# Kernel tuning notes

Measured on AMD Instinct MI355X. Metric: run time of the kernel, lower is better.

## Reference

```python
import jax, jax.numpy as jnp
import numpy as np

D_MODEL = 1024
NUM_HEADS = 16
D_K = D_MODEL // NUM_HEADS


def setup_inputs() -> dict:
    key = jax.random.key(0)
    ks = jax.random.split(key, 11)
    B, S = 4, 2048
    s = 1.0 / np.sqrt(D_MODEL)
    return {
        "query": jax.random.normal(ks[0], (B, S, D_MODEL), jnp.float32),
        "key_in": jax.random.normal(ks[1], (B, S, D_MODEL), jnp.float32),
        "value": jax.random.normal(ks[2], (B, S, D_MODEL), jnp.float32),
        "Wq": jax.random.normal(ks[3], (D_MODEL, D_MODEL), jnp.float32) * s,
        "bq": jnp.zeros((D_MODEL,), jnp.float32),
        "Wk": jax.random.normal(ks[4], (D_MODEL, D_MODEL), jnp.float32) * s,
        "bk": jnp.zeros((D_MODEL,), jnp.float32),
        "Wv": jax.random.normal(ks[5], (D_MODEL, D_MODEL), jnp.float32) * s,
        "bv": jnp.zeros((D_MODEL,), jnp.float32),
        "Wo": jax.random.normal(ks[6], (D_MODEL, D_MODEL), jnp.float32) * s,
        "bo": jnp.zeros((D_MODEL,), jnp.float32),
    }


def _split_heads(x):
    # (B, S, d_model) -> (B, H, S, d_k)
    B, S, _ = x.shape
    return x.reshape(B, S, NUM_HEADS, D_K).transpose(0, 2, 1, 3)


def reference(query, key_in, value, Wq, bq, Wk, bk, Wv, bv, Wo, bo):
    # Linear projections (torch nn.Linear: x @ W.T + b)
    Q = _split_heads(query @ Wq.T + bq)   # (B, H, Sq, d_k)
    K = _split_heads(key_in @ Wk.T + bk)  # (B, H, Sk, d_k)
    V = _split_heads(value @ Wv.T + bv)   # (B, H, Sk, d_k)
    # Scaled dot-product attention (mask=None path)
    scores = jnp.einsum('bhqd,bhkd->bhqk', Q, K) / jnp.sqrt(jnp.float32(D_K))
    attn = jax.nn.softmax(scores, axis=-1)
    out = jnp.einsum('bhqk,bhkd->bhqd', attn, V)  # (B, H, Sq, d_k)
    B, H, Sq, _ = out.shape
    out = out.transpose(0, 2, 1, 3).reshape(B, Sq, D_MODEL)
    return out @ Wo.T + bo
```

## Files before the change

kernel.cpp:

```cpp
#include <hip/hip_runtime.h>


#define DMODEL 1024
#define DK     64
#define NH     16
#define BSZ    4
#define SEQ    2048
#define MTOT   (BSZ * SEQ)

typedef __attribute__((ext_vector_type(8))) __bf16 bf16x8;
typedef __attribute__((ext_vector_type(4))) float  f32x4;

__device__ inline unsigned short f2bf(float x) {
    union { float f; unsigned u; } v; v.f = x;
    unsigned r = v.u + 0x7FFF + ((v.u >> 16) & 1u);
    return (unsigned short)(r >> 16);
}

__device__ inline bf16x8 ld_frag(const unsigned short* p) {
    return __builtin_bit_cast(bf16x8, *(const int4*)p);
}

union V8 { int4 v; unsigned short s[8]; };

__device__ inline void gload16(const unsigned short* g, unsigned short* l) {
    __builtin_amdgcn_global_load_lds(
        (const __attribute__((address_space(1))) void*)g,
        (__attribute__((address_space(3))) void*)l, 16, 0, 0);
}

__device__ inline unsigned pack_bf(float lo, float hi) {
    unsigned b0 = __builtin_bit_cast(unsigned, lo) + 0x8000u;
    unsigned b1 = __builtin_bit_cast(unsigned, hi) + 0x8000u;
    return __builtin_amdgcn_perm(b1, b0, 0x07060302u);
}

__global__ __launch_bounds__(256)
void conv_bf16(const float* __restrict__ src, unsigned short* __restrict__ dst)
{
    int i = blockIdx.x * 256 + threadIdx.x;
    const float4* s = (const float4*)src + (size_t)i * 2;
    float4 a = s[0], b = s[1];
    V8 u;
    u.s[0] = f2bf(a.x); u.s[1] = f2bf(a.y); u.s[2] = f2bf(a.z); u.s[3] = f2bf(a.w);
    u.s[4] = f2bf(b.x); u.s[5] = f2bf(b.y); u.s[6] = f2bf(b.z); u.s[7] = f2bf(b.w);
    ((int4*)dst)[i] = u.v;
}

template<int OUT_F32, int BIAS_ROW>
__global__ __launch_bounds__(256)
void gemm_bt16(const unsigned short* __restrict__ A, const unsigned short* __restrict__ Bt,
               const float* __restrict__ bias, void* __restrict__ Cout,
               int Mdim, int Ndim, int Kdim, float scale)
{
    __shared__ unsigned short As[128 * 64];
    __shared__ unsigned short Bs[128 * 64];

    const int tid  = threadIdx.x;
    const int wave = tid >> 6, lane = tid & 63, quad = lane >> 4, l16 = lane & 15;
    const int wm = wave >> 1, wn = wave & 1;
    const int m0 = blockIdx.x * 128, n0 = blockIdx.y * 128;

    const int srow = lane >> 3;
    const int pch  = lane & 7;

    f32x4 acc[4][4];
#pragma unroll
    for (int i = 0; i < 4; ++i)
#pragma unroll
        for (int j = 0; j < 4; ++j)
#pragma unroll
            for (int r = 0; r < 4; ++r) acc[i][j][r] = 0.f;

    for (int k0 = 0; k0 < Kdim; k0 += 64) {
#pragma unroll
        for (int rr = 0; rr < 4; ++rr) {
            int row = rr * 32 + wave * 8 + srow;
            int c   = pch ^ (row & 7);
            gload16(A + (size_t)(m0 + row) * Kdim + k0 + c * 8,
                    &As[(size_t)(rr * 32 + wave * 8) * 64]);
        }
#pragma unroll
        for (int rr = 0; rr < 4; ++rr) {
            int row = rr * 32 + wave * 8 + srow;
            int c   = pch ^ (row & 7);
            gload16(Bt + (size_t)(n0 + row) * Kdim + k0 + c * 8,
                    &Bs[(size_t)(rr * 32 + wave * 8) * 64]);
        }
        __syncthreads();

#pragma unroll
        for (int hh = 0; hh < 2; ++hh) {
            bf16x8 af[4], bfr[4];
#pragma unroll
            for (int t = 0; t < 4; ++t) {
                int ra = wm * 64 + t * 16 + l16;
                int pa = (hh * 4 + quad) ^ (l16 & 7);
                af[t] = ld_frag(&As[(size_t)ra * 64 + pa * 8]);
                int rb = wn * 64 + t * 16 + l16;
                bfr[t] = ld_frag(&Bs[(size_t)rb * 64 + pa * 8]);
            }
#pragma unroll
            for (int i = 0; i < 4; ++i)
#pragma unroll
                for (int j = 0; j < 4; ++j)
                    acc[i][j] = __builtin_amdgcn_mfma_f32_16x16x32_bf16(af[i], bfr[j], acc[i][j], 0, 0, 0);
        }
        __syncthreads();
    }

#pragma unroll
    for (int j = 0; j < 4; ++j) {
        int n = n0 + wn * 64 + j * 16 + l16;
        float bcol = BIAS_ROW ? 0.f : bias[n];
#pragma unroll
        for (int i = 0; i < 4; ++i) {
#pragma unroll
            for (int r = 0; r < 4; ++r) {
                int m = m0 + wm * 64 + i * 16 + quad * 4 + r;
                float bv = BIAS_ROW ? bias[m] : bcol;
                float val = (acc[i][j][r] + bv) * scale;
                if (OUT_F32) ((float*)Cout)[(size_t)m * Ndim + n] = val;
                else ((unsigned short*)Cout)[(size_t)m * Ndim + n] = f2bf(val);
            }
        }
    }
}

__global__ __launch_bounds__(256)
void attn_kernel(const unsigned short* __restrict__ Qb, const unsigned short* __restrict__ Kb,
                 const unsigned short* __restrict__ VbT, unsigned short* __restrict__ Ob)
{
    __shared__ unsigned short Ks[64 * 64];
    __shared__ unsigned short Vt[64 * 64];
    __shared__ unsigned short Ps[4][32][72];

    const int tid  = threadIdx.x;
    const int wave = tid >> 6, lane = tid & 63, quad = lane >> 4, l16 = lane & 15;
    const int q0 = blockIdx.x * 128, h = blockIdx.y, b = blockIdx.z;
    const int sw = l16 & 7;

    bf16x8 qf[2][2];
    const unsigned short* qbase = Qb + (size_t)(b * SEQ + q0 + wave * 32) * DMODEL + h * DK;
#pragma unroll
    for (int qs = 0; qs < 2; ++qs)
#pragma unroll
        for (int hh = 0; hh < 2; ++hh)
            qf[qs][hh] = ld_frag(qbase + (size_t)(qs * 16 + l16) * DMODEL + hh * 32 + quad * 8);

    f32x4 zero4;
#pragma unroll
    for (int r = 0; r < 4; ++r) zero4[r] = 0.f;

    f32x4 o[2][4], lacc[2];
#pragma unroll
    for (int qs = 0; qs < 2; ++qs) {
        lacc[qs] = zero4;
#pragma unroll
        for (int t = 0; t < 4; ++t) o[qs][t] = zero4;
    }

    bf16x8 onesf;
    {
        V8 u;
#pragma unroll
        for (int j = 0; j < 8; ++j) u.s[j] = 0x3F80;
        onesf = __builtin_bit_cast(bf16x8, u.v);
    }

    const int sr  = lane >> 3;
    const int pch = lane & 7;

    for (int kt = 0; kt < SEQ; kt += 64) {
        __syncthreads();
#pragma unroll
        for (int i = 0; i < 2; ++i) {
            int blk = wave * 2 + i;
            int row = blk * 8 + sr;
            int c   = pch ^ (row & 7);
            int key = 4 * (row & 15) + (row >> 4);
            gload16(Kb + (size_t)(b * SEQ + kt + key) * DMODEL + h * DK + c * 8,
                    &Ks[(size_t)blk * 512]);
            gload16(VbT + (size_t)(h * DK + row) * MTOT + b * SEQ + kt + c * 8,
                    &Vt[(size_t)blk * 512]);
        }
        __syncthreads();

        f32x4 s[2][4];
#pragma unroll
        for (int c = 0; c < 4; ++c) {
            bf16x8 kb0 = ld_frag(&Ks[(size_t)(c * 16 + l16) * 64 + ((quad ^ sw) * 8)]);
            bf16x8 kb1 = ld_frag(&Ks[(size_t)(c * 16 + l16) * 64 + (((4 + quad) ^ sw) * 8)]);
            s[0][c] = __builtin_amdgcn_mfma_f32_16x16x32_bf16(qf[0][1], kb1,
                      __builtin_amdgcn_mfma_f32_16x16x32_bf16(qf[0][0], kb0, zero4, 0, 0, 0), 0, 0, 0);
            s[1][c] = __builtin_amdgcn_mfma_f32_16x16x32_bf16(qf[1][1], kb1,
                      __builtin_amdgcn_mfma_f32_16x16x32_bf16(qf[1][0], kb0, zero4, 0, 0, 0), 0, 0, 0);
        }

#pragma unroll
        for (int qs = 0; qs < 2; ++qs)
#pragma unroll
            for (int r = 0; r < 4; ++r) {
                float p0 = __builtin_amdgcn_exp2f(s[qs][0][r]);
                float p1 = __builtin_amdgcn_exp2f(s[qs][1][r]);
                float p2 = __builtin_amdgcn_exp2f(s[qs][2][r]);
                float p3 = __builtin_amdgcn_exp2f(s[qs][3][r]);
                uint2 pk;
                pk.x = pack_bf(p0, p1);
                pk.y = pack_bf(p2, p3);
                *(uint2*)&Ps[wave][qs * 16 + quad * 4 + r][4 * l16] = pk;
            }

        bf16x8 pf[2][2];
#pragma unroll
        for (int qs = 0; qs < 2; ++qs)
#pragma unroll
            for (int hh = 0; hh < 2; ++hh)
                pf[qs][hh] = ld_frag(&Ps[wave][qs * 16 + l16][hh * 32 + quad * 8]);

#pragma unroll
        for (int qs = 0; qs < 2; ++qs) {
            lacc[qs] = __builtin_amdgcn_mfma_f32_16x16x32_bf16(pf[qs][0], onesf, lacc[qs], 0, 0, 0);
            lacc[qs] = __builtin_amdgcn_mfma_f32_16x16x32_bf16(pf[qs][1], onesf, lacc[qs], 0, 0, 0);
        }

#pragma unroll
        for (int t = 0; t < 4; ++t)
#pragma unroll
            for (int hh = 0; hh < 2; ++hh) {
                bf16x8 vb = ld_frag(&Vt[(size_t)(t * 16 + l16) * 64 + (((hh * 4 + quad) ^ sw) * 8)]);
                o[0][t] = __builtin_amdgcn_mfma_f32_16x16x32_bf16(pf[0][hh], vb, o[0][t], 0, 0, 0);
                o[1][t] = __builtin_amdgcn_mfma_f32_16x16x32_bf16(pf[1][hh], vb, o[1][t], 0, 0, 0);
            }
    }

#pragma unroll
    for (int qs = 0; qs < 2; ++qs) {
        float inv[4];
#pragma unroll
        for (int r = 0; r < 4; ++r) inv[r] = 1.f / lacc[qs][r];
#pragma unroll
        for (int t = 0; t < 4; ++t) {
            int d = h * DK + t * 16 + l16;
#pragma unroll
            for (int r = 0; r < 4; ++r) {
                int q = q0 + wave * 32 + qs * 16 + quad * 4 + r;
                Ob[(size_t)(b * SEQ + q) * DMODEL + d] = f2bf(o[qs][t][r] * inv[r]);
            }
        }
    }
}

extern "C" void kernel_launch(void* const* d_in, const int* in_sizes, int n_in,
                              void* d_out, int out_size, void* d_ws, size_t ws_size,
                              hipStream_t stream)
{
    const float* query  = (const float*)d_in[0];
    const float* key_in = (const float*)d_in[1];
    const float* value  = (const float*)d_in[2];
    const float* Wq = (const float*)d_in[3];
    const float* bq = (const float*)d_in[4];
    const float* Wk = (const float*)d_in[5];
    const float* bk = (const float*)d_in[6];
    const float* Wv = (const float*)d_in[7];
    const float* bv = (const float*)d_in[8];
    const float* Wo = (const float*)d_in[9];
    const float* bo = (const float*)d_in[10];

    const size_t NM = (size_t)MTOT * DMODEL;
    const size_t NW = (size_t)DMODEL * DMODEL;
    unsigned short* tmpA = (unsigned short*)d_ws;
    unsigned short* tmpW = tmpA + NM;
    unsigned short* Qb   = tmpW + NW;
    unsigned short* Kb   = Qb + NM;
    unsigned short* VbT  = Kb + NM;
    unsigned short* Ob   = tmpA;

    dim3 bb(256);
    const int gcA = (int)(NM / 8 / 256);
    const int gcW = (int)(NW / 8 / 256);
    dim3 gg(MTOT / 128, DMODEL / 128);
    dim3 gv(DMODEL / 128, MTOT / 128);

    const float qscale = 0.18033688f;

    conv_bf16<<<gcA, bb, 0, stream>>>(query, tmpA);
    conv_bf16<<<gcW, bb, 0, stream>>>(Wq, tmpW);
    gemm_bt16<0, 0><<<gg, bb, 0, stream>>>(tmpA, tmpW, bq, Qb, MTOT, DMODEL, DMODEL, qscale);

    conv_bf16<<<gcA, bb, 0, stream>>>(key_in, tmpA);
    conv_bf16<<<gcW, bb, 0, stream>>>(Wk, tmpW);
    gemm_bt16<0, 0><<<gg, bb, 0, stream>>>(tmpA, tmpW, bk, Kb, MTOT, DMODEL, DMODEL, 1.0f);

    conv_bf16<<<gcA, bb, 0, stream>>>(value, tmpA);
    conv_bf16<<<gcW, bb, 0, stream>>>(Wv, tmpW);
    gemm_bt16<0, 1><<<gv, bb, 0, stream>>>(tmpW, tmpA, bv, VbT, DMODEL, MTOT, DMODEL, 1.0f);

    attn_kernel<<<dim3(SEQ / 128, NH, BSZ), bb, 0, stream>>>(Qb, Kb, VbT, Ob);

    conv_bf16<<<gcW, bb, 0, stream>>>(Wo, tmpW);
    gemm_bt16<1, 0><<<gg, bb, 0, stream>>>(Ob, tmpW, bo, d_out, MTOT, DMODEL, DMODEL, 1.0f);
}
```

Baseline: 368.3 us.

## Batch QKV projections and conversions into single launches, retile output GEMM

Converts all three activations and all four weights to bf16 in two batched launches, keeping separate workspace buffers for each. The three projection GEMMs then run as one launch with blockIdx.z choosing Q, K or V, so 1536 blocks are in flight instead of 512 per launch. The output projection uses a 64x128 tile, giving twice as many blocks for better CU fill. This needs more workspace, so a fallback path keeps the old sequential launches when the workspace is too small.

```diff
diff --git a/kernel.cpp b/kernel.cpp
--- a/kernel.cpp
+++ b/kernel.cpp
@@ -35,10 +35,9 @@
     return __builtin_amdgcn_perm(b1, b0, 0x07060302u);
 }
 
-__global__ __launch_bounds__(256)
-void conv_bf16(const float* __restrict__ src, unsigned short* __restrict__ dst)
-{
-    int i = blockIdx.x * 256 + threadIdx.x;
+__device__ inline void conv_body(const float* __restrict__ src,
+                                 unsigned short* __restrict__ dst, int i)
+{
     const float4* s = (const float4*)src + (size_t)i * 2;
     float4 a = s[0], b = s[1];
     V8 u;
@@ -47,6 +46,35 @@
     ((int4*)dst)[i] = u.v;
 }
 
+__global__ __launch_bounds__(256)
+void conv_bf16(const float* __restrict__ src, unsigned short* __restrict__ dst)
+{
+    conv_body(src, dst, blockIdx.x * 256 + threadIdx.x);
+}
+
+__global__ __launch_bounds__(256)
+void conv3(const float* __restrict__ s0, const float* __restrict__ s1,
+           const float* __restrict__ s2, unsigned short* __restrict__ d0,
+           unsigned short* __restrict__ d1, unsigned short* __restrict__ d2)
+{
+    int z = blockIdx.z;
+    const float* s = (z == 0) ? s0 : (z == 1) ? s1 : s2;
+    unsigned short* d = (z == 0) ? d0 : (z == 1) ? d1 : d2;
+    conv_body(s, d, blockIdx.x * 256 + threadIdx.x);
+}
+
+__global__ __launch_bounds__(256)
+void conv4(const float* __restrict__ s0, const float* __restrict__ s1,
+           const float* __restrict__ s2, const float* __restrict__ s3,
+           unsigned short* __restrict__ d0, unsigned short* __restrict__ d1,
+           unsigned short* __restrict__ d2, unsigned short* __restrict__ d3)
+{
+    int z = blockIdx.z;
+    const float* s = (z == 0) ? s0 : (z == 1) ? s1 : (z == 2) ? s2 : s3;
+    unsigned short* d = (z == 0) ? d0 : (z == 1) ? d1 : (z == 2) ? d2 : d3;
+    conv_body(s, d, blockIdx.x * 256 + threadIdx.x);
+}
+
 template<int OUT_F32, int BIAS_ROW>
 __global__ __launch_bounds__(256)
 void gemm_bt16(const unsigned short* __restrict__ A, const unsigned short* __restrict__ Bt,
@@ -60,9 +88,7 @@
     const int wave = tid >> 6, lane = tid & 63, quad = lane >> 4, l16 = lane & 15;
     const int wm = wave >> 1, wn = wave & 1;
     const int m0 = blockIdx.x * 128, n0 = blockIdx.y * 128;
-
-    const int srow = lane >> 3;
-    const int pch  = lane & 7;
+    const int srow = lane >> 3, pch = lane & 7;
 
     f32x4 acc[4][4];
 #pragma unroll
@@ -122,6 +148,172 @@
                 float val = (acc[i][j][r] + bv) * scale;
                 if (OUT_F32) ((float*)Cout)[(size_t)m * Ndim + n] = val;
                 else ((unsigned short*)Cout)[(size_t)m * Ndim + n] = f2bf(val);
+            }
+        }
+    }
+}
+
+__global__ __launch_bounds__(256)
+void qkv_gemm(const unsigned short* __restrict__ Qa, const unsigned short* __restrict__ Ka,
+              const unsigned short* __restrict__ Va,
+              const unsigned short* __restrict__ Wqb, const unsigned short* __restrict__ Wkb,
+              const unsigned short* __restrict__ Wvb,
+              const float* __restrict__ bq, const float* __restrict__ bk,
+              const float* __restrict__ bv,
+              unsigned short* __restrict__ Qb, unsigned short* __restrict__ Kb,
+              unsigned short* __restrict__ VbT, float qscale)
+{
+    __shared__ unsigned short As[128 * 64];
+    __shared__ unsigned short Bs[128 * 64];
+
+    const int z = blockIdx.z;
+    const unsigned short* A  = (z == 0) ? Qa  : (z == 1) ? Ka  : Wvb;
+    const unsigned short* Bt = (z == 0) ? Wqb : (z == 1) ? Wkb : Va;
+    const float* bias        = (z == 0) ? bq  : (z == 1) ? bk  : bv;
+    unsigned short* out      = (z == 0) ? Qb  : (z == 1) ? Kb  : VbT;
+    const float scale  = (z == 0) ? qscale : 1.0f;
+    const int brow     = (z == 2);
+    const int m0       = brow ? blockIdx.y * 128 : blockIdx.x * 128;
+    const int n0       = brow ? blockIdx.x * 128 : blockIdx.y * 128;
+    const int ostride  = brow ? MTOT : DMODEL;
+
+    const int tid  = threadIdx.x;
+    const int wave = tid >> 6, lane = tid & 63, quad = lane >> 4, l16 = lane & 15;
+    const int wm = wave >> 1, wn = wave & 1;
+    const int srow = lane >> 3, pch = lane & 7;
+
+    f32x4 acc[4][4];
+#pragma unroll
+    for (int i = 0; i < 4; ++i)
+#pragma unroll
+        for (int j = 0; j < 4; ++j)
+#pragma unroll
+            for (int r = 0; r < 4; ++r) acc[i][j][r] = 0.f;
+
+    for (int k0 = 0; k0 < DMODEL; k0 += 64) {
+#pragma unroll
+        for (int rr = 0; rr < 4; ++rr) {
+            int row = rr * 32 + wave * 8 + srow;
+            int c   = pch ^ (row & 7);
+            gload16(A + (size_t)(m0 + row) * DMODEL + k0 + c * 8,
+                    &As[(size_t)(rr * 32 + wave * 8) * 64]);
+        }
+#pragma unroll
+        for (int rr = 0; rr < 4; ++rr) {
+            int row = rr * 32 + wave * 8 + srow;
+            int c   = pch ^ (row & 7);
+            gload16(Bt + (size_t)(n0 + row) * DMODEL + k0 + c * 8,
+                    &Bs[(size_t)(rr * 32 + wave * 8) * 64]);
+        }
+        __syncthreads();
+
+#pragma unroll
+        for (int hh = 0; hh < 2; ++hh) {
+            bf16x8 af[4], bfr[4];
+#pragma unroll
+            for (int t = 0; t < 4; ++t) {
+                int ra = wm * 64 + t * 16 + l16;
+                int pa = (hh * 4 + quad) ^ (l16 & 7);
+                af[t] = ld_frag(&As[(size_t)ra * 64 + pa * 8]);
+                int rb = wn * 64 + t * 16 + l16;
+                bfr[t] = ld_frag(&Bs[(size_t)rb * 64 + pa * 8]);
+            }
+#pragma unroll
+            for (int i = 0; i < 4; ++i)
+#pragma unroll
+                for (int j = 0; j < 4; ++j)
+                    acc[i][j] = __builtin_amdgcn_mfma_f32_16x16x32_bf16(af[i], bfr[j], acc[i][j], 0, 0, 0);
+        }
+        __syncthreads();
+    }
+
+#pragma unroll
+    for (int j = 0; j < 4; ++j) {
+        int n = n0 + wn * 64 + j * 16 + l16;
+        float bcol = brow ? 0.f : bias[n];
+#pragma unroll
+        for (int i = 0; i < 4; ++i) {
+#pragma unroll
+            for (int r = 0; r < 4; ++r) {
+                int m = m0 + wm * 64 + i * 16 + quad * 4 + r;
+                float bvv = brow ? bias[m] : bcol;
+                out[(size_t)m * ostride + n] = f2bf((acc[i][j][r] + bvv) * scale);
+            }
+        }
+    }
+}
+
+__global__ __launch_bounds__(256)
+void out_gemm(const unsigned short* __restrict__ A, const unsigned short* __restrict__ Bt,
+              const float* __restrict__ bias, float* __restrict__ C)
+{
+    __shared__ unsigned short As[64 * 64];
+    __shared__ unsigned short Bs[128 * 64];
+
+    const int tid  = threadIdx.x;
+    const int wave = tid >> 6, lane = tid & 63, quad = lane >> 4, l16 = lane & 15;
+    const int wm = wave >> 1, wn = wave & 1;
+    const int m0 = blockIdx.x * 64, n0 = blockIdx.y * 128;
+    const int srow = lane >> 3, pch = lane & 7;
+
+    f32x4 acc[2][4];
+#pragma unroll
+    for (int i = 0; i < 2; ++i)
+#pragma unroll
+        for (int j = 0; j < 4; ++j)
+#pragma unroll
+            for (int r = 0; r < 4; ++r) acc[i][j][r] = 0.f;
+
+    for (int k0 = 0; k0 < DMODEL; k0 += 64) {
+#pragma unroll
+        for (int rr = 0; rr < 2; ++rr) {
+            int row = rr * 32 + wave * 8 + srow;
+            int c   = pch ^ (row & 7);
+            gload16(A + (size_t)(m0 + row) * DMODEL + k0 + c * 8,
+                    &As[(size_t)(rr * 32 + wave * 8) * 64]);
+        }
+#pragma unroll
+        for (int rr = 0; rr < 4; ++rr) {
+            int row = rr * 32 + wave * 8 + srow;
+            int c   = pch ^ (row & 7);
+            gload16(Bt + (size_t)(n0 + row) * DMODEL + k0 + c * 8,
+                    &Bs[(size_t)(rr * 32 + wave * 8) * 64]);
+        }
+        __syncthreads();
+
+#pragma unroll
+        for (int hh = 0; hh < 2; ++hh) {
+            bf16x8 af[2], bfr[4];
+            int pa_base = hh * 4 + quad;
+#pragma unroll
+            for (int t = 0; t < 2; ++t) {
+                int ra = wm * 32 + t * 16 + l16;
+                af[t] = ld_frag(&As[(size_t)ra * 64 + ((pa_base ^ (l16 & 7)) * 8)]);
+            }
+#pragma unroll
+            for (int t = 0; t < 4; ++t) {
+                int rb = wn * 64 + t * 16 + l16;
+                bfr[t] = ld_frag(&Bs[(size_t)rb * 64 + ((pa_base ^ (l16 & 7)) * 8)]);
+            }
+#pragma unroll
+            for (int i = 0; i < 2; ++i)
+#pragma unroll
+                for (int j = 0; j < 4; ++j)
+                    acc[i][j] = __builtin_amdgcn_mfma_f32_16x16x32_bf16(af[i], bfr[j], acc[i][j], 0, 0, 0);
+        }
+        __syncthreads();
+    }
+
+#pragma unroll
+    for (int j = 0; j < 4; ++j) {
+        int n = n0 + wn * 64 + j * 16 + l16;
+        float bcol = bias[n];
+#pragma unroll
+        for (int i = 0; i < 2; ++i) {
+#pragma unroll
+            for (int r = 0; r < 4; ++r) {
+                int m = m0 + wm * 32 + i * 16 + quad * 4 + r;
+                C[(size_t)m * DMODEL + n] = acc[i][j][r] + bcol;
             }
         }
     }
@@ -269,35 +461,61 @@
 
     const size_t NM = (size_t)MTOT * DMODEL;
     const size_t NW = (size_t)DMODEL * DMODEL;
-    unsigned short* tmpA = (unsigned short*)d_ws;
-    unsigned short* tmpW = tmpA + NM;
-    unsigned short* Qb   = tmpW + NW;
-    unsigned short* Kb   = Qb + NM;
-    unsigned short* VbT  = Kb + NM;
-    unsigned short* Ob   = tmpA;
-
+    const float qscale = 0.18033688f;
     dim3 bb(256);
-    const int gcA = (int)(NM / 8 / 256);
-    const int gcW = (int)(NW / 8 / 256);
-    dim3 gg(MTOT / 128, DMODEL / 128);
-    dim3 gv(DMODEL / 128, MTOT / 128);
-
-    const float qscale = 0.18033688f;
-
-    conv_bf16<<<gcA, bb, 0, stream>>>(query, tmpA);
-    conv_bf16<<<gcW, bb, 0, stream>>>(Wq, tmpW);
-    gemm_bt16<0, 0><<<gg, bb, 0, stream>>>(tmpA, tmpW, bq, Qb, MTOT, DMODEL, DMODEL, qscale);
-
-    conv_bf16<<<gcA, bb, 0, stream>>>(key_in, tmpA);
-    conv_bf16<<<gcW, bb, 0, stream>>>(Wk, tmpW);
-    gemm_bt16<0, 0><<<gg, bb, 0, stream>>>(tmpA, tmpW, bk, Kb, MTOT, DMODEL, DMODEL, 1.0f);
-
-    conv_bf16<<<gcA, bb, 0, stream>>>(value, tmpA);
-    conv_bf16<<<gcW, bb, 0, stream>>>(Wv, tmpW);
-    gemm_bt16<0, 1><<<gv, bb, 0, stream>>>(tmpW, tmpA, bv, VbT, DMODEL, MTOT, DMODEL, 1.0f);
-
-    attn_kernel<<<dim3(SEQ / 128, NH, BSZ), bb, 0, stream>>>(Qb, Kb, VbT, Ob);
-
-    conv_bf16<<<gcW, bb, 0, stream>>>(Wo, tmpW);
-    gemm_bt16<1, 0><<<gg, bb, 0, stream>>>(Ob, tmpW, bo, d_out, MTOT, DMODEL, DMODEL, 1.0f);
-}
+
+    const size_t need_primary = (6 * NM + 4 * NW) * 2;
+
+    if (ws_size >= need_primary) {
+        unsigned short* Qa  = (unsigned short*)d_ws;
+        unsigned short* Ka  = Qa + NM;
+        unsigned short* Va  = Ka + NM;
+        unsigned short* Qb  = Va + NM;
+        unsigned short* Kb  = Qb + NM;
+        unsigned short* VbT = Kb + NM;
+        unsigned short* Wqb = VbT + NM;
+        unsigned short* Wkb = Wqb + NW;
+        unsigned short* Wvb = Wkb + NW;
+        unsigned short* Wob = Wvb + NW;
+        unsigned short* Ob  = Qa;
+
+        conv3<<<dim3(4096, 1, 3), bb, 0, stream>>>(query, key_in, value, Qa, Ka, Va);
+        conv4<<<dim3(512, 1, 4), bb, 0, stream>>>(Wq, Wk, Wv, Wo, Wqb, Wkb, Wvb, Wob);
+
+        qkv_gemm<<<dim3(MTOT / 128, DMODEL / 128, 3), bb, 0, stream>>>(
+            Qa, Ka, Va, Wqb, Wkb, Wvb, bq, bk, bv, Qb, Kb, VbT, qscale);
+
+        attn_kernel<<<dim3(SEQ / 128, NH, BSZ), bb, 0, stream>>>(Qb, Kb, VbT, Ob);
+
+        out_gemm<<<dim3(MTOT / 64, DMODEL / 128), bb, 0, stream>>>(Ob, Wob, bo, (float*)d_out);
+    } else {
+        unsigned short* tmpA = (unsigned short*)d_ws;
+        unsigned short* tmpW = tmpA + NM;
+        unsigned short* Qb   = tmpW + NW;
+        unsigned short* Kb   = Qb + NM;
+        unsigned short* VbT  = Kb + NM;
+        unsigned short* Ob   = tmpA;
+
+        const int gcA = (int)(NM / 8 / 256);
+        const int gcW = (int)(NW / 8 / 256);
+        dim3 gg(MTOT / 128, DMODEL / 128);
+        dim3 gv(DMODEL / 128, MTOT / 128);
+
+        conv_bf16<<<gcA, bb, 0, stream>>>(query, tmpA);
+        conv_bf16<<<gcW, bb, 0, stream>>>(Wq, tmpW);
+        gemm_bt16<0, 0><<<gg, bb, 0, stream>>>(tmpA, tmpW, bq, Qb, MTOT, DMODEL, DMODEL, qscale);
+
+        conv_bf16<<<gcA, bb, 0, stream>>>(key_in, tmpA);
+        conv_bf16<<<gcW, bb, 0, stream>>>(Wk, tmpW);
+        gemm_bt16<0, 0><<<gg, bb, 0, stream>>>(tmpA, tmpW, bk, Kb, MTOT, DMODEL, DMODEL, 1.0f);
+
+        conv_bf16<<<gcA, bb, 0, stream>>>(value, tmpA);
+        conv_bf16<<<gcW, bb, 0, stream>>>(Wv, tmpW);
+        gemm_bt16<0, 1><<<gv, bb, 0, stream>>>(tmpW, tmpA, bv, VbT, DMODEL, MTOT, DMODEL, 1.0f);
+
+        attn_kernel<<<dim3(SEQ / 128, NH, BSZ), bb, 0, stream>>>(Qb, Kb, VbT, Ob);
+
+        conv_bf16<<<gcW, bb, 0, stream>>>(Wo, tmpW);
+        out_gemm<<<dim3(MTOT / 64, DMODEL / 128), bb, 0, stream>>>(Ob, tmpW, bo, (float*)d_out);
+    }
+}
```

Result: no change. 369.6 us (+0.3%).
